# Kernel tuning notes

Hardware: AMD Instinct MI355X
Metric: run time of the kernel (lower is better)

Reference implementation:

```python
import jax, jax.numpy as jnp
import numpy as np

N_NODES = 100000
N_EDGES = 3200000
D_IN = 128
D_OUT = 128


def setup_inputs() -> dict:
    key = jax.random.key(0)
    k1, k2, k3 = jax.random.split(key, 3)
    x = jax.random.normal(k1, (N_NODES, D_IN), dtype=jnp.float32)
    W = jax.random.normal(k2, (D_OUT, D_IN), dtype=jnp.float32) * (1.0 / np.sqrt(D_IN))
    edge_index = jax.random.randint(k3, (2, N_EDGES), 0, N_NODES, dtype=jnp.int32)
    return {"x": x, "W": W, "edge_index": edge_index}


def reference(x, W, edge_index):
    # Linear without bias: h = x @ W^T  (torch Linear convention)
    h = x @ W.T  # [N, D_OUT]
    # Sparse adjacency matmul: out[i] = sum_{j : (j->i) in E} h[j]
    src = edge_index[0]
    dst = edge_index[1]
    msgs = h[src]  # gather [E, D_OUT]
    out = jax.ops.segment_sum(msgs, dst, num_segments=N_NODES)
    return out
```

## Files before the change

kernel.cpp:

```cpp
#include <hip/hip_runtime.h>

#define D 128
#define PSHIFT 9
#define PCAP 17664
#define SDEPTH 48
#define NP_MAX 256
#define NBF 768
#define BCAP 2560
#define CHUNK 2048
#define OW 136

typedef __attribute__((ext_vector_type(8))) short short8;
typedef __attribute__((ext_vector_type(4))) float f32x4;

__device__ __forceinline__ unsigned short f2bf(float f) {
    union { float f; unsigned int u; } c; c.f = f;
    unsigned int b = c.u;
    unsigned int r = (b + 0x7FFFu + ((b >> 16) & 1u)) >> 16;
    return (unsigned short)r;
}
__device__ __forceinline__ float bf2f(unsigned short s) {
    union { unsigned int u; float f; } c; c.u = ((unsigned int)s) << 16;
    return c.f;
}

__global__ void k_init(int* __restrict__ gcur, int np, int* __restrict__ bcur, int nb) {
    int i = blockIdx.x * 256 + threadIdx.x;
    if (i < np) gcur[i << 4] = i * PCAP;
    if (i < nb) bcur[i << 4] = i * BCAP;
}

__global__ __launch_bounds__(256) void k_prep(const float* __restrict__ W,
                                              unsigned short* __restrict__ whl) {
    const int i = blockIdx.x * 256 + threadIdx.x;
    if (i >= (D * D / 8)) return;
    const int o = i >> 4;
    const int gk = i & 15;
    const float* wp = W + o * D + gk * 8;
    float4 a0 = *(const float4*)wp;
    float4 a1 = *(const float4*)(wp + 4);
    float v[8] = {a0.x, a0.y, a0.z, a0.w, a1.x, a1.y, a1.z, a1.w};
    unsigned short hi[8], lo[8];
#pragma unroll
    for (int j = 0; j < 8; j++) {
        hi[j] = f2bf(v[j]);
        lo[j] = f2bf(v[j] - bf2f(hi[j]));
    }
    const int base = o * D + ((gk ^ (o & 7)) << 3);
    ushort4 h0 = {hi[0], hi[1], hi[2], hi[3]};
    ushort4 h1 = {hi[4], hi[5], hi[6], hi[7]};
    ushort4 l0 = {lo[0], lo[1], lo[2], lo[3]};
    ushort4 l1 = {lo[4], lo[5], lo[6], lo[7]};
    *(ushort4*)&whl[base] = h0;
    *(ushort4*)&whl[base + 4] = h1;
    *(ushort4*)&whl[16384 + base] = l0;
    *(ushort4*)&whl[16384 + base + 4] = l1;
}

__global__ __launch_bounds__(256, 2) void k_gemm_mfma(const float* __restrict__ x,
                                                      const unsigned short* __restrict__ whl,
                                                      unsigned short* __restrict__ h,
                                                      int N) {
    __shared__ unsigned short sbuf[2 * 16384];

    const int t = threadIdx.x;

    {
        const float4* g4 = (const float4*)whl;
        float4* l4 = (float4*)sbuf;
#pragma unroll
        for (int i = 0; i < 16; i++) l4[t + i * 256] = g4[t + i * 256];
    }
    __syncthreads();

    const int lane = t & 63;
    const int wv = t >> 6;
    const int lr = lane & 15;
    const int lg = lane >> 4;
    const int rowbase = blockIdx.x * 128 + wv * 32;

    float4 xr[2][4][2];
#pragma unroll
    for (int rg = 0; rg < 2; rg++) {
        const int row = rowbase + rg * 16 + lr;
        const float* xp = x + (size_t)row * D + lg * 8;
        const bool ok = (row < N);
#pragma unroll
        for (int ks = 0; ks < 4; ks++) {
            xr[rg][ks][0] = ok ? *(const float4*)(xp + ks * 32) : make_float4(0.f, 0.f, 0.f, 0.f);
            xr[rg][ks][1] = ok ? *(const float4*)(xp + ks * 32 + 4) : make_float4(0.f, 0.f, 0.f, 0.f);
        }
    }

    f32x4 acc[2][8];
#pragma unroll
    for (int a = 0; a < 2; a++)
#pragma unroll
        for (int b = 0; b < 8; b++)
            acc[a][b] = (f32x4){0.f, 0.f, 0.f, 0.f};

#pragma unroll
    for (int ks = 0; ks < 4; ks++) {
        short8 ah[2], al[2];
#pragma unroll
        for (int rg = 0; rg < 2; rg++) {
            float v[8] = {xr[rg][ks][0].x, xr[rg][ks][0].y, xr[rg][ks][0].z, xr[rg][ks][0].w,
                          xr[rg][ks][1].x, xr[rg][ks][1].y, xr[rg][ks][1].z, xr[rg][ks][1].w};
#pragma unroll
            for (int j = 0; j < 8; j++) {
                unsigned short hj = f2bf(v[j]);
                ah[rg][j] = (short)hj;
                al[rg][j] = (short)f2bf(v[j] - bf2f(hj));
            }
        }
#pragma unroll
        for (int tt = 0; tt < 8; tt++) {
            const int o = tt * 16 + lr;
            const int eoff = o * D + ((((ks << 2) + lg) ^ (lr & 7)) << 3);
            short8 bh = *(const short8*)&sbuf[eoff];
            short8 bl = *(const short8*)&sbuf[16384 + eoff];
#pragma unroll
            for (int rg = 0; rg < 2; rg++) {
                acc[rg][tt] = __builtin_amdgcn_mfma_f32_16x16x32_bf16(ah[rg], bh, acc[rg][tt], 0, 0, 0);
                acc[rg][tt] = __builtin_amdgcn_mfma_f32_16x16x32_bf16(al[rg], bh, acc[rg][tt], 0, 0, 0);
                acc[rg][tt] = __builtin_amdgcn_mfma_f32_16x16x32_bf16(ah[rg], bl, acc[rg][tt], 0, 0, 0);
            }
        }
    }

    __syncthreads();
#pragma unroll
    for (int rg = 0; rg < 2; rg++)
#pragma unroll
        for (int i2 = 0; i2 < 4; i2++) {
            const int row = wv * 32 + rg * 16 + lg * 4 + i2;
#pragma unroll
            for (int tt = 0; tt < 8; tt++)
                sbuf[row * OW + tt * 16 + lr] = f2bf(acc[rg][tt][i2]);
        }
    __syncthreads();
#pragma unroll
    for (int it = 0; it < 8; it++) {
        const int idx = t + it * 256;
        const int row = idx >> 4;
        const int seg = idx & 15;
        const int grow = blockIdx.x * 128 + row;
        if (grow < N)
            *(short8*)(h + (size_t)grow * D + seg * 8) =
                *(const short8*)&sbuf[row * OW + seg * 8];
    }
}

__global__ __launch_bounds__(256) void k_bin1(const int* __restrict__ src,
                                              const int* __restrict__ dst,
                                              int* __restrict__ gcur,
                                              unsigned* __restrict__ packed,
                                              int E, int np, int epb) {
    __shared__ unsigned stage[NP_MAX * SDEPTH];
    __shared__ int scnt[NP_MAX];

    const int t = threadIdx.x;
    for (int i = t; i < np; i += 256) scnt[i] = 0;
    __syncthreads();

    const int beg = blockIdx.x * epb;
    const int end = min(beg + epb, E);
    for (int e = beg + t; e < end; e += 256) {
        const int d = dst[e];
        const int s = src[e];
        const int p = d >> PSHIFT;
        const unsigned entry = (unsigned)s | ((unsigned)(d & ((1 << PSHIFT) - 1)) << 17);
        const int slot = atomicAdd(&scnt[p], 1);
        if (slot < SDEPTH) {
            stage[p * SDEPTH + slot] = entry;
        } else {
            const int pos = atomicAdd(&gcur[p << 4], 1);
            if (pos - p * PCAP < PCAP) packed[pos] = entry;
        }
    }
    __syncthreads();

    for (int i = t; i < np; i += 256) {
        const int c = min(scnt[i], SDEPTH);
        if (c) {
            const int base = atomicAdd(&gcur[i << 4], c);
            const int lim = (i + 1) * PCAP;
            for (int j = 0; j < c; j++) {
                const int pos = base + j;
                if (pos < lim) packed[pos] = stage[i * SDEPTH + j];
            }
        }
    }
}

__global__ __launch_bounds__(256) void k_bin2(const unsigned* __restrict__ packed,
                                              const int* __restrict__ gcur,
                                              int* __restrict__ bcur,
                                              unsigned* __restrict__ bslab,
                                              int np) {
    __shared__ unsigned raw[CHUNK];
    __shared__ unsigned srt[CHUNK];
    __shared__ int c8[8], o8[9], cur8[8], gbase[8];

    const int p = blockIdx.x >> 2;
    const int qb = blockIdx.x & 3;
    const int t = threadIdx.x;

    const int base = p * PCAP;
    const int sz = min(gcur[p << 4] - base, PCAP);
    const int per = (sz + 3) >> 2;
    const int rbeg = qb * per;
    const int rend = min(rbeg + per, sz);
    const unsigned* pk = packed + (size_t)base;

    for (int cbeg = rbeg; cbeg < rend; cbeg += CHUNK) {
        const int n = min(CHUNK, rend - cbeg);
        for (int i = t; i < n; i += 256) raw[i] = pk[cbeg + i];
        if (t < 8) c8[t] = 0;
        __syncthreads();
        for (int i = t; i < n; i += 256) atomicAdd(&c8[raw[i] >> 23], 1);
        __syncthreads();
        if (t == 0) {
            int s = 0;
#pragma unroll
            for (int j = 0; j < 8; j++) { o8[j] = s; s += c8[j]; }
            o8[8] = s;
        }
        __syncthreads();
        if (t < 8) {
            cur8[t] = o8[t];
            gbase[t] = atomicAdd(&bcur[(p * 8 + t) << 4], c8[t]);
        }
        __syncthreads();
        for (int i = t; i < n; i += 256) {
            const unsigned e = raw[i];
            const int pos = atomicAdd(&cur8[e >> 23], 1);
            srt[pos] = e & 0x7FFFFFu;
        }
        __syncthreads();
#pragma unroll
        for (int b = 0; b < 8; b++) {
            const int cnt = o8[b + 1] - o8[b];
            const int gb = gbase[b];
            const int lim = (p * 8 + b + 1) * BCAP;
            const int m2 = min(cnt, max(0, lim - gb));
            for (int i = t; i < m2; i += 256) bslab[gb + i] = srt[o8[b] + i];
        }
        __syncthreads();
    }
}

__global__ __launch_bounds__(256) void k_gather(const unsigned short* __restrict__ h,
                                                const unsigned* __restrict__ bslab,
                                                const int* __restrict__ bcur,
                                                float* __restrict__ out, int N) {
    __shared__ unsigned lsrc[BCAP];
    __shared__ int cnt[256];
    __shared__ int off[257];
    __shared__ int curs[256];

    const int bk = blockIdx.x;
    const int t = threadIdx.x;
    const int hw = t >> 5;
    const int f = (t & 31) << 2;

    const int sz = min(bcur[bk << 4] - bk * BCAP, BCAP);
    const unsigned* pk = bslab + (size_t)bk * BCAP;

    cnt[t] = 0;
    __syncthreads();
    for (int i = t; i < sz; i += 256)
        atomicAdd(&cnt[(pk[i] >> 15) & 255u], 1);
    __syncthreads();
    if (t == 0) {
        int s = 0;
        for (int j = 0; j < 256; j++) { off[j] = s; s += cnt[j]; }
        off[256] = s;
    }
    __syncthreads();
    curs[t] = off[t];
    __syncthreads();
    for (int i = t; i < sz; i += 256) {
        unsigned p = pk[i];
        int pos = atomicAdd(&curs[(p >> 15) & 255u], 1);
        lsrc[pos] = p & 0x1FFFFu;
    }
    __syncthreads();

    float4 acc[8];
#pragma unroll
    for (int r = 0; r < 8; r++) acc[r] = make_float4(0.f, 0.f, 0.f, 0.f);

    for (int q = 0; q < 4; q++) {
#pragma unroll
        for (int r = 0; r < 8; r++) {
            const int nl = hw + (r << 3);
            const int idx = (nl << 2) + q;
            int j = off[idx];
            const int je = off[idx + 1];
            float4 a = acc[r];
            for (; j + 3 < je; j += 4) {
                int s0 = lsrc[j], s1 = lsrc[j + 1], s2 = lsrc[j + 2], s3 = lsrc[j + 3];
                ushort4 v0 = *(const ushort4*)(h + (size_t)s0 * D + f);
                ushort4 v1 = *(const ushort4*)(h + (size_t)s1 * D + f);
                ushort4 v2 = *(const ushort4*)(h + (size_t)s2 * D + f);
                ushort4 v3 = *(const ushort4*)(h + (size_t)s3 * D + f);
                a.x += bf2f(v0.x) + bf2f(v1.x) + bf2f(v2.x) + bf2f(v3.x);
                a.y += bf2f(v0.y) + bf2f(v1.y) + bf2f(v2.y) + bf2f(v3.y);
                a.z += bf2f(v0.z) + bf2f(v1.z) + bf2f(v2.z) + bf2f(v3.z);
                a.w += bf2f(v0.w) + bf2f(v1.w) + bf2f(v2.w) + bf2f(v3.w);
            }
            for (; j < je; j++) {
                int s0 = lsrc[j];
                ushort4 v0 = *(const ushort4*)(h + (size_t)s0 * D + f);
                a.x += bf2f(v0.x); a.y += bf2f(v0.y);
                a.z += bf2f(v0.z); a.w += bf2f(v0.w);
            }
            acc[r] = a;
        }
    }

#pragma unroll
    for (int r = 0; r < 8; r++) {
        int node = (bk << 6) + hw + (r << 3);
        if (node < N) *(float4*)(out + (size_t)node * D + f) = acc[r];
    }
}

extern "C" void kernel_launch(void* const* d_in, const int* in_sizes, int n_in,
                              void* d_out, int out_size, void* d_ws, size_t ws_size,
                              hipStream_t stream) {
    const float* x = (const float*)d_in[0];
    const float* W = (const float*)d_in[1];
    const int* ei  = (const int*)d_in[2];
    float* out = (float*)d_out;

    const int N = in_sizes[0] / D;
    const int E = in_sizes[2] / 2;
    const int np = (N + 511) >> PSHIFT;
    const int nb = (N + 63) >> 6;
    const int epb = (E + NBF - 1) / NBF;

    const int* srcp = ei;
    const int* dstp = ei + E;

    char* ws = (char*)d_ws;
    unsigned short* h = (unsigned short*)ws;
                                      ws += (size_t)N * D * 2;
    unsigned* packed = (unsigned*)ws; ws += (size_t)np * PCAP * 4;
    unsigned* bslab = (unsigned*)ws;  ws += (size_t)nb * BCAP * 4;
    unsigned short* whl = (unsigned short*)ws;
                                      ws += (size_t)2 * 16384 * 2;
    int* gcur = (int*)ws;             ws += (size_t)np * 64;
    int* bcur = (int*)ws;             ws += (size_t)nb * 64;

    k_init<<<(nb + 255) / 256, 256, 0, stream>>>(gcur, np, bcur, nb);
    k_prep<<<8, 256, 0, stream>>>(W, whl);
    k_gemm_mfma<<<(N + 127) / 128, 256, 0, stream>>>(x, whl, h, N);
    k_bin1<<<NBF, 256, 0, stream>>>(srcp, dstp, gcur, packed, E, np, epb);
    k_bin2<<<np * 4, 256, 0, stream>>>(packed, gcur, bcur, bslab, np);
    k_gather<<<nb, 256, 0, stream>>>(h, bslab, bcur, out, N);
}
```

Before: 273.1 us.

## Widen gather blocks to 512 threads, parallelize bucket scan, merge setup kernels

The gather kernel now runs 512 threads per block. Each half-wave handles 4 destination nodes instead of 8, which halves per-thread accumulator state and serial work. The single-thread 256-entry prefix sum over bucket counts is replaced by a wavefront shuffle scan plus a tiny 4-element serial combine, cutting serialized LDS work before the gather phase. The separate init and weight-prep kernels are merged into one launch to save launch overhead, at the cost of slightly more register pressure and larger blocks in the gather kernel.

Result: no change. 272.1 us (-0.4%).

```diff
diff --git a/kernel.cpp b/kernel.cpp
--- a/kernel.cpp
+++ b/kernel.cpp
@@ -24,37 +24,36 @@
     return c.f;
 }
 
-__global__ void k_init(int* __restrict__ gcur, int np, int* __restrict__ bcur, int nb) {
-    int i = blockIdx.x * 256 + threadIdx.x;
+__global__ __launch_bounds__(256) void k_setup(const float* __restrict__ W,
+                                               unsigned short* __restrict__ whl,
+                                               int* __restrict__ gcur, int np,
+                                               int* __restrict__ bcur, int nb) {
+    const int i = blockIdx.x * 256 + threadIdx.x;
     if (i < np) gcur[i << 4] = i * PCAP;
     if (i < nb) bcur[i << 4] = i * BCAP;
-}
-
-__global__ __launch_bounds__(256) void k_prep(const float* __restrict__ W,
-                                              unsigned short* __restrict__ whl) {
-    const int i = blockIdx.x * 256 + threadIdx.x;
-    if (i >= (D * D / 8)) return;
-    const int o = i >> 4;
-    const int gk = i & 15;
-    const float* wp = W + o * D + gk * 8;
-    float4 a0 = *(const float4*)wp;
-    float4 a1 = *(const float4*)(wp + 4);
-    float v[8] = {a0.x, a0.y, a0.z, a0.w, a1.x, a1.y, a1.z, a1.w};
-    unsigned short hi[8], lo[8];
-#pragma unroll
-    for (int j = 0; j < 8; j++) {
-        hi[j] = f2bf(v[j]);
-        lo[j] = f2bf(v[j] - bf2f(hi[j]));
-    }
-    const int base = o * D + ((gk ^ (o & 7)) << 3);
-    ushort4 h0 = {hi[0], hi[1], hi[2], hi[3]};
-    ushort4 h1 = {hi[4], hi[5], hi[6], hi[7]};
-    ushort4 l0 = {lo[0], lo[1], lo[2], lo[3]};
-    ushort4 l1 = {lo[4], lo[5], lo[6], lo[7]};
-    *(ushort4*)&whl[base] = h0;
-    *(ushort4*)&whl[base + 4] = h1;
-    *(ushort4*)&whl[16384 + base] = l0;
-    *(ushort4*)&whl[16384 + base + 4] = l1;
+    if (i < (D * D / 8)) {
+        const int o = i >> 4;
+        const int gk = i & 15;
+        const float* wp = W + o * D + gk * 8;
+        float4 a0 = *(const float4*)wp;
+        float4 a1 = *(const float4*)(wp + 4);
+        float v[8] = {a0.x, a0.y, a0.z, a0.w, a1.x, a1.y, a1.z, a1.w};
+        unsigned short hi[8], lo[8];
+#pragma unroll
+        for (int j = 0; j < 8; j++) {
+            hi[j] = f2bf(v[j]);
+            lo[j] = f2bf(v[j] - bf2f(hi[j]));
+        }
+        const int base = o * D + ((gk ^ (o & 7)) << 3);
+        ushort4 h0 = {hi[0], hi[1], hi[2], hi[3]};
+        ushort4 h1 = {hi[4], hi[5], hi[6], hi[7]};
+        ushort4 l0 = {lo[0], lo[1], lo[2], lo[3]};
+        ushort4 l1 = {lo[4], lo[5], lo[6], lo[7]};
+        *(ushort4*)&whl[base] = h0;
+        *(ushort4*)&whl[base + 4] = h1;
+        *(ushort4*)&whl[16384 + base] = l0;
+        *(ushort4*)&whl[16384 + base + 4] = l1;
+    }
 }
 
 __global__ __launch_bounds__(256, 2) void k_gemm_mfma(const float* __restrict__ x,
@@ -250,7 +249,7 @@
     }
 }
 
-__global__ __launch_bounds__(256) void k_gather(const unsigned short* __restrict__ h,
+__global__ __launch_bounds__(512) void k_gather(const unsigned short* __restrict__ h,
                                                 const unsigned* __restrict__ bslab,
                                                 const int* __restrict__ bcur,
                                                 float* __restrict__ out, int N) {
@@ -258,6 +257,7 @@
     __shared__ int cnt[256];
     __shared__ int off[257];
     __shared__ int curs[256];
+    __shared__ int wpart[4];
 
     const int bk = blockIdx.x;
     const int t = threadIdx.x;
@@ -267,34 +267,55 @@
     const int sz = min(bcur[bk << 4] - bk * BCAP, BCAP);
     const unsigned* pk = bslab + (size_t)bk * BCAP;
 
-    cnt[t] = 0;
-    __syncthreads();
-    for (int i = t; i < sz; i += 256)
+    if (t < 256) cnt[t] = 0;
+    __syncthreads();
+    for (int i = t; i < sz; i += 512)
         atomicAdd(&cnt[(pk[i] >> 15) & 255u], 1);
+    __syncthreads();
+
+    const int lane = t & 63;
+    const int w = t >> 6;
+    int c = 0, v = 0;
+    if (t < 256) {
+        c = cnt[t];
+        v = c;
+#pragma unroll
+        for (int d2 = 1; d2 < 64; d2 <<= 1) {
+            int up = __shfl_up(v, d2, 64);
+            if (lane >= d2) v += up;
+        }
+        if (lane == 63) wpart[w] = v;
+    }
     __syncthreads();
     if (t == 0) {
         int s = 0;
-        for (int j = 0; j < 256; j++) { off[j] = s; s += cnt[j]; }
+#pragma unroll
+        for (int j2 = 0; j2 < 4; j2++) { const int x2 = wpart[j2]; wpart[j2] = s; s += x2; }
         off[256] = s;
     }
     __syncthreads();
-    curs[t] = off[t];
-    __syncthreads();
-    for (int i = t; i < sz; i += 256) {
+    if (t < 256) {
+        const int e = v - c + wpart[w];
+        off[t] = e;
+        curs[t] = e;
+    }
+    __syncthreads();
+
+    for (int i = t; i < sz; i += 512) {
         unsigned p = pk[i];
         int pos = atomicAdd(&curs[(p >> 15) & 255u], 1);
         lsrc[pos] = p & 0x1FFFFu;
     }
     __syncthreads();
 
-    float4 acc[8];
-#pragma unroll
-    for (int r = 0; r < 8; r++) acc[r] = make_float4(0.f, 0.f, 0.f, 0.f);
+    float4 acc[4];
+#pragma unroll
+    for (int r = 0; r < 4; r++) acc[r] = make_float4(0.f, 0.f, 0.f, 0.f);
 
     for (int q = 0; q < 4; q++) {
 #pragma unroll
-        for (int r = 0; r < 8; r++) {
-            const int nl = hw + (r << 3);
+        for (int r = 0; r < 4; r++) {
+            const int nl = hw + (r << 4);
             const int idx = (nl << 2) + q;
             int j = off[idx];
             const int je = off[idx + 1];
@@ -321,8 +342,8 @@
     }
 
 #pragma unroll
-    for (int r = 0; r < 8; r++) {
-        int node = (bk << 6) + hw + (r << 3);
+    for (int r = 0; r < 4; r++) {
+        const int node = (bk << 6) + hw + (r << 4);
         if (node < N) *(float4*)(out + (size_t)node * D + f) = acc[r];
     }
 }
@@ -354,10 +375,9 @@
     int* gcur = (int*)ws;             ws += (size_t)np * 64;
     int* bcur = (int*)ws;             ws += (size_t)nb * 64;
 
-    k_init<<<(nb + 255) / 256, 256, 0, stream>>>(gcur, np, bcur, nb);
-    k_prep<<<8, 256, 0, stream>>>(W, whl);
+    k_setup<<<8, 256, 0, stream>>>(W, whl, gcur, np, bcur, nb);
     k_gemm_mfma<<<(N + 127) / 128, 256, 0, stream>>>(x, whl, h, N);
     k_bin1<<<NBF, 256, 0, stream>>>(srcp, dstp, gcur, packed, E, np, epb);
     k_bin2<<<np * 4, 256, 0, stream>>>(packed, gcur, bcur, bslab, np);
-    k_gather<<<nb, 256, 0, stream>>>(h, bslab, bcur, out, N);
-}
+    k_gather<<<nb, 512, 0, stream>>>(h, bslab, bcur, out, N);
+}
```
